# Optimization experiments

Hardware: AMD Instinct MI355X
Metric: run time of the kernel (lower is better)

The kernel has to match this reference:

```python
import jax, jax.numpy as jnp
import numpy as np

B, T, C = 4, 2048, 1024
NH = 16
HD = C // NH


def setup_inputs() -> dict:
    key = jax.random.key(0)
    ks = jax.random.split(key, 5)
    s = 0.02
    return {
        "x": jax.random.normal(ks[0], (B, T, C), dtype=jnp.float32),
        "w_attn": jax.random.normal(ks[1], (C, 3 * C), dtype=jnp.float32) * s,
        "b_attn": jnp.zeros((3 * C,), dtype=jnp.float32),
        "w_proj": jax.random.normal(ks[2], (C, C), dtype=jnp.float32) * s,
        "b_proj": jnp.zeros((C,), dtype=jnp.float32),
    }


def reference(x, w_attn, b_attn, w_proj, b_proj):
    Bx, Tx, Cx = x.shape
    qkv = x @ w_attn + b_attn                       # [B,T,3C]
    q, k, v = jnp.split(qkv, 3, axis=-1)
    # [B,T,C] -> [B,NH,T,HD]
    def heads(t):
        return t.reshape(Bx, Tx, NH, HD).transpose(0, 2, 1, 3)
    q, k, v = heads(q), heads(k), heads(v)
    scale = HD ** -0.5
    attn = jnp.einsum("bhqd,bhkd->bhqk", q, k) * scale
    causal = jnp.tril(jnp.ones((Tx, Tx), dtype=bool))
    attn = jnp.where(causal[None, None], attn, -jnp.inf)
    attn = jax.nn.softmax(attn, axis=-1)
    out = jnp.einsum("bhqk,bhkd->bhqd", attn, v)    # [B,NH,T,HD]
    out = out.transpose(0, 2, 1, 3).reshape(Bx, Tx, Cx)
    return out @ w_proj + b_proj
```

## Files before the change

### kernel.cpp

```cpp
#include <hip/hip_runtime.h>
#include <hip/hip_bf16.h>
#include <stdint.h>

using f32x4  = __attribute__((ext_vector_type(4))) float;
using bf16x8 = __attribute__((ext_vector_type(8))) short;
using u16x4  = __attribute__((ext_vector_type(4))) ushort;

#define MFMA16(a, b, c) __builtin_amdgcn_mfma_f32_16x16x32_bf16((a), (b), (c), 0, 0, 0)

__device__ __forceinline__ void gload_lds16(const void* g, void* l) {
    __builtin_amdgcn_global_load_lds(
        (const __attribute__((address_space(1))) void*)g,
        (__attribute__((address_space(3))) void*)l, 16, 0, 0);
}

__device__ __forceinline__ ushort f2bf(float f) {
    union { float f; uint32_t u; } v; v.f = f;
    uint32_t r = v.u + 0x7fffu + ((v.u >> 16) & 1u);
    return (ushort)(r >> 16);
}
__device__ __forceinline__ float bf2f(ushort u) {
    union { uint32_t u; float f; } v; v.u = ((uint32_t)u) << 16;
    return v.f;
}
__device__ __forceinline__ uint32_t pk_bf16(float a, float b) {
    __hip_bfloat162 h = __float22bfloat162_rn(float2{a, b});
    union { __hip_bfloat162 h; uint32_t u; } v; v.h = h; return v.u;
}
__device__ __forceinline__ bf16x8 scale8(bf16x8 v, float s) {
    bf16x8 r;
#pragma unroll
    for (int j = 0; j < 8; ++j) r[j] = (short)f2bf(bf2f((ushort)v[j]) * s);
    return r;
}

#define NEG_BIG (-1.0e30f)

__global__ void pack_bf16_k(const float* __restrict__ in, ushort* __restrict__ out, int n4) {
    const int i = blockIdx.x * blockDim.x + threadIdx.x;
    if (i >= n4) return;
    const f32x4 v = *(const f32x4*)(in + (size_t)i * 4);
    u16x4 o;
    o[0] = f2bf(v[0]); o[1] = f2bf(v[1]); o[2] = f2bf(v[2]); o[3] = f2bf(v[3]);
    *(u16x4*)(out + (size_t)i * 4) = o;
}

__global__ void transpose_k(const float* __restrict__ in, ushort* __restrict__ out,
                            int R, int C) {
    __shared__ ushort tile[32][33];
    const int c0 = blockIdx.x * 32, r0 = blockIdx.y * 32;
    const int tx = threadIdx.x, ty = threadIdx.y;
    for (int i = ty; i < 32; i += 8)
        tile[i][tx] = f2bf(in[(size_t)(r0 + i) * C + c0 + tx]);
    __syncthreads();
    for (int i = ty; i < 32; i += 8)
        out[(size_t)(c0 + i) * R + r0 + tx] = tile[tx][i];
}

template <int MODE>
__global__ __launch_bounds__(256, 2)
void gemm_bt(const ushort* __restrict__ A, const ushort* __restrict__ BT,
             const float* __restrict__ bias, float* __restrict__ outF,
             ushort* __restrict__ qk, ushort* __restrict__ vt,
             int M, int N, int K) {
    __shared__ __align__(16) ushort As[128 * 32];
    __shared__ __align__(16) ushort Bs[128 * 32];
    const int tid  = threadIdx.x;
    const int lane = tid & 63;
    const int wid  = tid >> 6;
    const int l15  = lane & 15, lg = lane >> 4;
    const int tile_m = blockIdx.x * 128;
    const int tile_n = blockIdx.y * 128;
    const int wm = (wid >> 1) * 64;
    const int wn = (wid & 1) * 64;

    const f32x4 fzero = {0.f, 0.f, 0.f, 0.f};
    f32x4 acc[4][4];
#pragma unroll
    for (int i = 0; i < 4; ++i)
#pragma unroll
        for (int j = 0; j < 4; ++j) acc[i][j] = fzero;

    const int c0 = tid & 3;
    const int r0 = tid >> 2;
    const ushort* Arow0 = A  + (size_t)(tile_m + r0)      * K + c0 * 8;
    const ushort* Arow1 = A  + (size_t)(tile_m + 64 + r0) * K + c0 * 8;
    const ushort* Brow0 = BT + (size_t)(tile_n + r0)      * K + c0 * 8;
    const ushort* Brow1 = BT + (size_t)(tile_n + 64 + r0) * K + c0 * 8;
    const int ldsb0 = (wid * 64) * 16;
    const int ldsb1 = (256 + wid * 64) * 16;

    for (int k0 = 0; k0 < K; k0 += 32) {
        gload_lds16(Arow0 + k0, (char*)As + ldsb0);
        gload_lds16(Arow1 + k0, (char*)As + ldsb1);
        gload_lds16(Brow0 + k0, (char*)Bs + ldsb0);
        gload_lds16(Brow1 + k0, (char*)Bs + ldsb1);
        __syncthreads();

        bf16x8 af[4], bfv[4];
#pragma unroll
        for (int mf = 0; mf < 4; ++mf)
            af[mf] = *(const bf16x8*)&As[(wm + mf * 16 + l15) * 32 + lg * 8];
#pragma unroll
        for (int nf = 0; nf < 4; ++nf)
            bfv[nf] = *(const bf16x8*)&Bs[(wn + nf * 16 + l15) * 32 + lg * 8];
#pragma unroll
        for (int mf = 0; mf < 4; ++mf)
#pragma unroll
            for (int nf = 0; nf < 4; ++nf)
                acc[mf][nf] = MFMA16(af[mf], bfv[nf], acc[mf][nf]);
        __syncthreads();
    }

#pragma unroll
    for (int nf = 0; nf < 4; ++nf) {
        const int col = tile_n + wn + nf * 16 + l15;
        const float bv = bias[col];
#pragma unroll
        for (int mf = 0; mf < 4; ++mf) {
#pragma unroll
            for (int i = 0; i < 4; ++i) {
                const int row = tile_m + wm + mf * 16 + lg * 4 + i;
                const float val = acc[mf][nf][i] + bv;
                if (MODE == 0) {
                    outF[(size_t)row * N + col] = val;
                } else {
                    if (col < 2048) {
                        qk[(size_t)row * 2048 + col] = f2bf(val);
                    } else {
                        const int vc = col - 2048;
                        const int bb = row >> 11, t = row & 2047;
                        vt[((size_t)(bb * 16 + (vc >> 6)) * 64 + (vc & 63)) * 2048 + t] = f2bf(val);
                    }
                }
            }
        }
    }
}

__global__ __launch_bounds__(256)
void attn_fwd(const ushort* __restrict__ qk, const ushort* __restrict__ vt,
              ushort* __restrict__ ao) {
    const int tid  = threadIdx.x;
    const int lane = tid & 63;
    const int w    = tid >> 6;
    const int l15  = lane & 15, lg = lane >> 4;
    const int bh = blockIdx.y;
    const int b = bh >> 4, h = bh & 15;

    __shared__ __align__(16) ushort Ks[2][64 * 64];
    __shared__ __align__(16) ushort Vs[2][64 * 64];
    __shared__ __align__(16) ushort Ps[4][32 * 80];

    char* psw = (char*)&Ps[w][0];
    const int pswz = (l15 & 7) << 4;

    const ushort* kbase = qk + (size_t)b * 2048 * 2048 + 1024 + h * 64;
    const ushort* vbase = vt + (size_t)bh * 64 * 2048;
    const float sscale = 0.125f * 1.4426950408889634f;

    const int srow0 = tid >> 3,        schk0 = (tid & 7) ^ (srow0 & 7);
    const int srow1 = (256 + tid) >> 3, schk1 = (tid & 7) ^ (srow1 & 7);

    for (int pass = 0; pass < 2; ++pass) {
        const int q0 = (pass ? (15 - blockIdx.x) : blockIdx.x) * 128;
        const int qw = q0 + w * 32;

        const ushort* qrow = qk + ((size_t)(b * 2048 + qw + l15)) * 2048 + h * 64 + lg * 8;
        bf16x8 qf[2][2];
        qf[0][0] = scale8(*(const bf16x8*)(qrow), sscale);
        qf[0][1] = scale8(*(const bf16x8*)(qrow + 32), sscale);
        qf[1][0] = scale8(*(const bf16x8*)(qrow + 16 * 2048), sscale);
        qf[1][1] = scale8(*(const bf16x8*)(qrow + 16 * 2048 + 32), sscale);

        const f32x4 fzero = {0.f, 0.f, 0.f, 0.f};
        f32x4 o[2][4];
#pragma unroll
        for (int qh = 0; qh < 2; ++qh)
#pragma unroll
            for (int f = 0; f < 4; ++f) o[qh][f] = fzero;
        float mrun[2] = {NEG_BIG, NEG_BIG};
        float lrun[2] = {0.f, 0.f};

        const int nt = q0 / 64 + 2;

        {
            gload_lds16(kbase + (size_t)srow0 * 2048 + schk0 * 8, (char*)Ks[0] + tid * 16);
            gload_lds16(kbase + (size_t)srow1 * 2048 + schk1 * 8, (char*)Ks[0] + (256 + tid) * 16);
            gload_lds16(vbase + (size_t)srow0 * 2048 + schk0 * 8, (char*)Vs[0] + tid * 16);
            gload_lds16(vbase + (size_t)srow1 * 2048 + schk1 * 8, (char*)Vs[0] + (256 + tid) * 16);
        }
        __syncthreads();

        for (int t = 0; t < nt; ++t) {
            const int cur = t & 1;
            const int kv0 = t * 64;
            if (t + 1 < nt) {
                const int nkv = kv0 + 64;
                ushort* kd = Ks[cur ^ 1];
                ushort* vd = Vs[cur ^ 1];
                gload_lds16(kbase + (size_t)(nkv + srow0) * 2048 + schk0 * 8, (char*)kd + tid * 16);
                gload_lds16(kbase + (size_t)(nkv + srow1) * 2048 + schk1 * 8, (char*)kd + (256 + tid) * 16);
                gload_lds16(vbase + (size_t)srow0 * 2048 + nkv + schk0 * 8, (char*)vd + tid * 16);
                gload_lds16(vbase + (size_t)srow1 * 2048 + nkv + schk1 * 8, (char*)vd + (256 + tid) * 16);
            }

            if (kv0 <= qw + 31) {
                const char* kls = (const char*)Ks[cur];
                const char* vls = (const char*)Vs[cur];

                bf16x8 kf[4][2];
#pragma unroll
                for (int hh = 0; hh < 4; ++hh)
#pragma unroll
                    for (int dc = 0; dc < 2; ++dc)
                        kf[hh][dc] = *(const bf16x8*)(kls + (hh * 16 + l15) * 128 +
                                                      (((dc * 4 + lg) ^ (l15 & 7)) << 4));

#pragma unroll
                for (int qh = 0; qh < 2; ++qh) {
                    if (kv0 > qw + qh * 16 + 15) continue;
                    f32x4 st[4] = {fzero, fzero, fzero, fzero};
#pragma unroll
                    for (int hh = 0; hh < 4; ++hh)
#pragma unroll
                        for (int dc = 0; dc < 2; ++dc)
                            st[hh] = MFMA16(kf[hh][dc], qf[qh][dc], st[hh]);

                    float p[16];
#pragma unroll
                    for (int hh = 0; hh < 4; ++hh)
#pragma unroll
                        for (int i = 0; i < 4; ++i) p[hh * 4 + i] = st[hh][i];
                    if (kv0 + 63 > qw + qh * 16) {
                        const int qg = qw + qh * 16 + l15;
#pragma unroll
                        for (int hh = 0; hh < 4; ++hh)
#pragma unroll
                            for (int i = 0; i < 4; ++i) {
                                const int kvg = kv0 + hh * 16 + lg * 4 + i;
                                if (kvg > qg) p[hh * 4 + i] = NEG_BIG;
                            }
                    }

                    float mt = p[0];
#pragma unroll
                    for (int j = 1; j < 16; ++j) mt = fmaxf(mt, p[j]);
                    mt = fmaxf(mt, __shfl_xor(mt, 16));
                    mt = fmaxf(mt, __shfl_xor(mt, 32));

                    if (!__all(mt <= mrun[qh])) {
                        const float mn = fmaxf(mrun[qh], mt);
                        const float alpha = exp2f(mrun[qh] - mn);
                        mrun[qh] = mn;
                        float ar[4];
#pragma unroll
                        for (int i = 0; i < 4; ++i) ar[i] = __shfl(alpha, lg * 4 + i);
#pragma unroll
                        for (int f = 0; f < 4; ++f)
#pragma unroll
                            for (int i = 0; i < 4; ++i) o[qh][f][i] *= ar[i];
                        lrun[qh] *= alpha;
                    }

                    float rs = 0.f;
#pragma unroll
                    for (int j = 0; j < 16; ++j) { p[j] = exp2f(p[j] - mrun[qh]); rs += p[j]; }
                    rs += __shfl_xor(rs, 16);
                    rs += __shfl_xor(rs, 32);
                    lrun[qh] += rs;

                    const int prow = qh * 16 + l15;
#pragma unroll
                    for (int hh = 0; hh < 4; ++hh) {
                        uint2 pk;
                        pk.x = pk_bf16(p[hh * 4 + 0], p[hh * 4 + 1]);
                        pk.y = pk_bf16(p[hh * 4 + 2], p[hh * 4 + 3]);
                        *(uint2*)(psw + ((prow * 160 + hh * 32 + lg * 8) ^ pswz)) = pk;
                    }
                }

                bf16x8 pf[2][2];
#pragma unroll
                for (int qh = 0; qh < 2; ++qh)
#pragma unroll
                    for (int ks = 0; ks < 2; ++ks)
                        pf[qh][ks] = *(const bf16x8*)(psw + (((qh * 16 + l15) * 160 + ks * 64 + lg * 16) ^ pswz));

#pragma unroll
                for (int f = 0; f < 4; ++f) {
                    const int vrow = f * 16 + l15;
                    bf16x8 vf0 = *(const bf16x8*)(vls + vrow * 128 + ((lg ^ (l15 & 7)) << 4));
                    bf16x8 vf1 = *(const bf16x8*)(vls + vrow * 128 + (((4 + lg) ^ (l15 & 7)) << 4));
#pragma unroll
                    for (int qh = 0; qh < 2; ++qh) {
                        if (kv0 > qw + qh * 16 + 15) continue;
                        o[qh][f] = MFMA16(pf[qh][0], vf0, o[qh][f]);
                        o[qh][f] = MFMA16(pf[qh][1], vf1, o[qh][f]);
                    }
                }
            }
            __syncthreads();
        }

#pragma unroll
        for (int qh = 0; qh < 2; ++qh) {
            float lr[4];
#pragma unroll
            for (int i = 0; i < 4; ++i) lr[i] = __shfl(lrun[qh], lg * 4 + i);
#pragma unroll
            for (int f = 0; f < 4; ++f)
#pragma unroll
                for (int i = 0; i < 4; ++i) {
                    const int row = qw + qh * 16 + lg * 4 + i;
                    const int col = h * 64 + f * 16 + l15;
                    ao[((size_t)(b * 2048 + row)) * 1024 + col] = f2bf(o[qh][f][i] / lr[i]);
                }
        }
    }
}

extern "C" void kernel_launch(void* const* d_in, const int* in_sizes, int n_in,
                              void* d_out, int out_size, void* d_ws, size_t ws_size,
                              hipStream_t stream) {
    const float* x      = (const float*)d_in[0];
    const float* w_attn = (const float*)d_in[1];
    const float* b_attn = (const float*)d_in[2];
    const float* w_proj = (const float*)d_in[3];
    const float* b_proj = (const float*)d_in[4];
    float* out = (float*)d_out;

    ushort* ws  = (ushort*)d_ws;
    ushort* xb  = ws;
    ushort* wTa = xb  + (size_t)8192 * 1024;
    ushort* wTp = wTa + (size_t)3072 * 1024;
    ushort* qkb = wTp + (size_t)1024 * 1024;
    ushort* vtb = qkb + (size_t)8192 * 2048;
    ushort* aob = vtb + (size_t)64 * 64 * 2048;
    const size_t needed = ((size_t)8192 * 1024 + (size_t)3072 * 1024 + (size_t)1024 * 1024 +
                           (size_t)8192 * 2048 + (size_t)64 * 64 * 2048 + (size_t)8192 * 1024) * 2;
    if (ws_size < needed) return;

    pack_bf16_k<<<8192, 256, 0, stream>>>(x, xb, 8192 * 1024 / 4);
    transpose_k<<<dim3(96, 32), dim3(32, 8), 0, stream>>>(w_attn, wTa, 1024, 3072);
    transpose_k<<<dim3(32, 32), dim3(32, 8), 0, stream>>>(w_proj, wTp, 1024, 1024);
    gemm_bt<1><<<dim3(64, 24), 256, 0, stream>>>(xb, wTa, b_attn, nullptr, qkb, vtb, 8192, 3072, 1024);
    attn_fwd<<<dim3(8, 64), 256, 0, stream>>>(qkb, vtb, aob);
    gemm_bt<0><<<dim3(64, 8), 256, 0, stream>>>(aob, wTp, b_proj, out, nullptr, nullptr, 8192, 1024, 1024);
}
```

Before: 323.1 us.

## Rewrite GEMMs with 256x256 tiles, double-buffered LDS and swizzled layout

Replaces the 128x128 single-buffered GEMM with a 256x256-tile, 512-thread kernel that double-buffers K-slices of 64 in LDS. Loads go straight to LDS, waits use explicit vmcnt, and an XOR swizzle avoids bank conflicts. Blocks are remapped so neighbouring blocks share tiles in L2, and the V-transpose stores are packed into 8-byte writes. Each block now keeps more accumulators in registers and uses 128KB of LDS, which may cut occupancy. The projection GEMM drops to 128 blocks, which may leave compute units idle.

```diff
diff --git a/kernel.cpp b/kernel.cpp
--- a/kernel.cpp
+++ b/kernel.cpp
@@ -33,6 +33,14 @@
     for (int j = 0; j < 8; ++j) r[j] = (short)f2bf(bf2f((ushort)v[j]) * s);
     return r;
 }
+
+__device__ __forceinline__ void wgbar() {
+    asm volatile("" ::: "memory");
+    __builtin_amdgcn_s_barrier();
+    asm volatile("" ::: "memory");
+}
+#define VMW8 asm volatile("s_waitcnt vmcnt(8)" ::: "memory")
+#define VMW0 asm volatile("s_waitcnt vmcnt(0)" ::: "memory")
 
 #define NEG_BIG (-1.0e30f)
 
@@ -58,58 +66,86 @@
 }
 
 template <int MODE>
-__global__ __launch_bounds__(256, 2)
-void gemm_bt(const ushort* __restrict__ A, const ushort* __restrict__ BT,
+__global__ __launch_bounds__(512, 2)
+void gemm256(const ushort* __restrict__ A, const ushort* __restrict__ BT,
              const float* __restrict__ bias, float* __restrict__ outF,
              ushort* __restrict__ qk, ushort* __restrict__ vt,
-             int M, int N, int K) {
-    __shared__ __align__(16) ushort As[128 * 32];
-    __shared__ __align__(16) ushort Bs[128 * 32];
+             int N, int K) {
+    __shared__ __align__(16) ushort As[2][256 * 64];
+    __shared__ __align__(16) ushort Bs[2][256 * 64];
     const int tid  = threadIdx.x;
     const int lane = tid & 63;
     const int wid  = tid >> 6;
     const int l15  = lane & 15, lg = lane >> 4;
-    const int tile_m = blockIdx.x * 128;
-    const int tile_n = blockIdx.y * 128;
-    const int wm = (wid >> 1) * 64;
-    const int wn = (wid & 1) * 64;
+    const int wm = (wid >> 2) * 128;
+    const int wn = (wid & 3) * 64;
+
+    const int cpx = gridDim.x >> 3;
+    const int swz = (blockIdx.x & 7) * cpx + (blockIdx.x >> 3);
+    const int tile_m = (swz & 31) << 8;
+    const int tile_n = (swz >> 5) << 8;
 
     const f32x4 fzero = {0.f, 0.f, 0.f, 0.f};
-    f32x4 acc[4][4];
-#pragma unroll
-    for (int i = 0; i < 4; ++i)
+    f32x4 acc[8][4];
+#pragma unroll
+    for (int i = 0; i < 8; ++i)
 #pragma unroll
         for (int j = 0; j < 4; ++j) acc[i][j] = fzero;
 
-    const int c0 = tid & 3;
-    const int r0 = tid >> 2;
-    const ushort* Arow0 = A  + (size_t)(tile_m + r0)      * K + c0 * 8;
-    const ushort* Arow1 = A  + (size_t)(tile_m + 64 + r0) * K + c0 * 8;
-    const ushort* Brow0 = BT + (size_t)(tile_n + r0)      * K + c0 * 8;
-    const ushort* Brow1 = BT + (size_t)(tile_n + 64 + r0) * K + c0 * 8;
-    const int ldsb0 = (wid * 64) * 16;
-    const int ldsb1 = (256 + wid * 64) * 16;
-
-    for (int k0 = 0; k0 < K; k0 += 32) {
-        gload_lds16(Arow0 + k0, (char*)As + ldsb0);
-        gload_lds16(Arow1 + k0, (char*)As + ldsb1);
-        gload_lds16(Brow0 + k0, (char*)Bs + ldsb0);
-        gload_lds16(Brow1 + k0, (char*)Bs + ldsb1);
-        __syncthreads();
-
-        bf16x8 af[4], bfv[4];
-#pragma unroll
-        for (int mf = 0; mf < 4; ++mf)
-            af[mf] = *(const bf16x8*)&As[(wm + mf * 16 + l15) * 32 + lg * 8];
-#pragma unroll
-        for (int nf = 0; nf < 4; ++nf)
-            bfv[nf] = *(const bf16x8*)&Bs[(wn + nf * 16 + l15) * 32 + lg * 8];
-#pragma unroll
-        for (int mf = 0; mf < 4; ++mf)
-#pragma unroll
-            for (int nf = 0; nf < 4; ++nf)
-                acc[mf][nf] = MFMA16(af[mf], bfv[nf], acc[mf][nf]);
-        __syncthreads();
+    const ushort* aP[4]; const ushort* bP[4]; int dOff[4];
+#pragma unroll
+    for (int i = 0; i < 4; ++i) {
+        const int c = i * 512 + tid;
+        const int row = c >> 3;
+        const int ch = (c & 7) ^ (row & 7);
+        aP[i] = A  + (size_t)(tile_m + row) * K + ch * 8;
+        bP[i] = BT + (size_t)(tile_n + row) * K + ch * 8;
+        dOff[i] = c * 16;
+    }
+
+    auto STAGE = [&](int buf, int kt) {
+        const int k0 = kt * 64;
+#pragma unroll
+        for (int i = 0; i < 4; ++i) gload_lds16(aP[i] + k0, (char*)As[buf] + dOff[i]);
+#pragma unroll
+        for (int i = 0; i < 4; ++i) gload_lds16(bP[i] + k0, (char*)Bs[buf] + dOff[i]);
+    };
+
+    auto COMPUTE = [&](int buf) {
+        const char* Ab = (const char*)As[buf];
+        const char* Bb = (const char*)Bs[buf];
+#pragma unroll
+        for (int kk = 0; kk < 2; ++kk) {
+            bf16x8 a[8], b[4];
+#pragma unroll
+            for (int mf = 0; mf < 8; ++mf) {
+                const int row = wm + mf * 16 + l15;
+                a[mf] = *(const bf16x8*)(Ab + row * 128 + ((((kk << 2) + lg) ^ (row & 7)) << 4));
+            }
+#pragma unroll
+            for (int nf = 0; nf < 4; ++nf) {
+                const int row = wn + nf * 16 + l15;
+                b[nf] = *(const bf16x8*)(Bb + row * 128 + ((((kk << 2) + lg) ^ (row & 7)) << 4));
+            }
+#pragma unroll
+            for (int mf = 0; mf < 8; ++mf)
+#pragma unroll
+                for (int nf = 0; nf < 4; ++nf)
+                    acc[mf][nf] = MFMA16(a[mf], b[nf], acc[mf][nf]);
+        }
+    };
+
+    const int nt = K >> 6;
+    STAGE(0, 0);
+    STAGE(1, 1);
+    int cur = 0;
+    for (int t = 0; t < nt; ++t) {
+        if (t < nt - 1) { VMW8; } else { VMW0; }
+        wgbar();
+        COMPUTE(cur);
+        wgbar();
+        if (t + 2 < nt) STAGE(cur, t + 2);
+        cur ^= 1;
     }
 
 #pragma unroll
@@ -117,21 +153,26 @@
         const int col = tile_n + wn + nf * 16 + l15;
         const float bv = bias[col];
 #pragma unroll
-        for (int mf = 0; mf < 4; ++mf) {
-#pragma unroll
-            for (int i = 0; i < 4; ++i) {
-                const int row = tile_m + wm + mf * 16 + lg * 4 + i;
-                const float val = acc[mf][nf][i] + bv;
-                if (MODE == 0) {
-                    outF[(size_t)row * N + col] = val;
+        for (int mf = 0; mf < 8; ++mf) {
+            const int row = tile_m + wm + mf * 16 + lg * 4;
+            float v0 = acc[mf][nf][0] + bv, v1 = acc[mf][nf][1] + bv;
+            float v2 = acc[mf][nf][2] + bv, v3 = acc[mf][nf][3] + bv;
+            if (MODE == 0) {
+                outF[(size_t)(row + 0) * N + col] = v0;
+                outF[(size_t)(row + 1) * N + col] = v1;
+                outF[(size_t)(row + 2) * N + col] = v2;
+                outF[(size_t)(row + 3) * N + col] = v3;
+            } else {
+                if (col < 2048) {
+                    qk[(size_t)(row + 0) * 2048 + col] = f2bf(v0);
+                    qk[(size_t)(row + 1) * 2048 + col] = f2bf(v1);
+                    qk[(size_t)(row + 2) * 2048 + col] = f2bf(v2);
+                    qk[(size_t)(row + 3) * 2048 + col] = f2bf(v3);
                 } else {
-                    if (col < 2048) {
-                        qk[(size_t)row * 2048 + col] = f2bf(val);
-                    } else {
-                        const int vc = col - 2048;
-                        const int bb = row >> 11, t = row & 2047;
-                        vt[((size_t)(bb * 16 + (vc >> 6)) * 64 + (vc & 63)) * 2048 + t] = f2bf(val);
-                    }
+                    const int vc = col - 2048;
+                    const int bb = row >> 11, t = row & 2047;
+                    uint2 w; w.x = pk_bf16(v0, v1); w.y = pk_bf16(v2, v3);
+                    *(uint2*)(vt + ((size_t)(bb * 16 + (vc >> 6)) * 64 + (vc & 63)) * 2048 + t) = w;
                 }
             }
         }
@@ -159,7 +200,7 @@
     const ushort* vbase = vt + (size_t)bh * 64 * 2048;
     const float sscale = 0.125f * 1.4426950408889634f;
 
-    const int srow0 = tid >> 3,        schk0 = (tid & 7) ^ (srow0 & 7);
+    const int srow0 = tid >> 3,         schk0 = (tid & 7) ^ (srow0 & 7);
     const int srow1 = (256 + tid) >> 3, schk1 = (tid & 7) ^ (srow1 & 7);
 
     for (int pass = 0; pass < 2; ++pass) {
@@ -344,7 +385,7 @@
     pack_bf16_k<<<8192, 256, 0, stream>>>(x, xb, 8192 * 1024 / 4);
     transpose_k<<<dim3(96, 32), dim3(32, 8), 0, stream>>>(w_attn, wTa, 1024, 3072);
     transpose_k<<<dim3(32, 32), dim3(32, 8), 0, stream>>>(w_proj, wTp, 1024, 1024);
-    gemm_bt<1><<<dim3(64, 24), 256, 0, stream>>>(xb, wTa, b_attn, nullptr, qkb, vtb, 8192, 3072, 1024);
+    gemm256<1><<<384, 512, 0, stream>>>(xb, wTa, b_attn, nullptr, qkb, vtb, 3072, 1024);
     attn_fwd<<<dim3(8, 64), 256, 0, stream>>>(qkb, vtb, aob);
-    gemm_bt<0><<<dim3(64, 8), 256, 0, stream>>>(aob, wTp, b_proj, out, nullptr, nullptr, 8192, 1024, 1024);
-}
+    gemm256<0><<<128, 512, 0, stream>>>(aob, wTp, b_proj, out, nullptr, nullptr, 1024, 1024);
+}
```

After: 330.3 us. 2.2% more time.
